# Optimization experiments

Measured on AMD Instinct MI355X. Metric: run time of the kernel, lower is better.

The kernel has to match this reference:

```python
import jax, jax.numpy as jnp
import numpy as np

ALPHA = 1.702
LIMIT = 7.0
BLOCK = 32  # mxfp4 block size (values per scale)

# fp4 e2m1 lookup table, indexed by 4-bit code (sign in high bit)
FP4_LUT = jnp.array([0.0, 0.5, 1.0, 1.5, 2.0, 3.0, 4.0, 6.0,
                     -0.0, -0.5, -1.0, -1.5, -2.0, -3.0, -4.0, -6.0],
                    dtype=jnp.float32)


def dequant_mxfp4(blocks, scales):
    # blocks: [E, R, C//2] int byte values (two fp4 nibbles per byte, low nibble first)
    # scales: [E, R, C//32] e8m0 exponents; value = 2^(scale - 127)
    E, R, _ = blocks.shape
    nb = scales.shape[-1]
    lo = blocks & 0xF
    hi = (blocks >> 4) & 0xF
    vals = jnp.stack([FP4_LUT[lo], FP4_LUT[hi]], axis=-1)  # [E,R,C//2,2]
    vals = vals.reshape(E, R, nb, BLOCK)
    scale = jnp.exp2((scales - 127).astype(jnp.float32))   # [E,R,nb]
    return (vals * scale[..., None]).reshape(E, R, nb * BLOCK)  # [E,R,C]


def setup_inputs() -> dict:
    key = jax.random.key(0)
    ks = jax.random.split(key, 12)
    T, E, H, I = 1024, 8, 1024, 1024
    inp = {
        'hidden_states': jax.random.normal(ks[0], (T, H), dtype=jnp.float32),
        'router_logits': jax.random.normal(ks[1], (T, E), dtype=jnp.float32),
        'gate_proj_blocks': jax.random.randint(ks[2], (E, I, H // 2), 0, 256, dtype=jnp.int32),
        'gate_proj_scales': jax.random.randint(ks[3], (E, I, H // BLOCK), 121, 130, dtype=jnp.int32),
        'gate_proj_bias': jax.random.normal(ks[4], (E, I), dtype=jnp.float32) * 0.02,
        'up_proj_blocks': jax.random.randint(ks[5], (E, I, H // 2), 0, 256, dtype=jnp.int32),
        'up_proj_scales': jax.random.randint(ks[6], (E, I, H // BLOCK), 121, 130, dtype=jnp.int32),
        'up_proj_bias': jax.random.normal(ks[7], (E, I), dtype=jnp.float32) * 0.02,
        'down_proj_blocks': jax.random.randint(ks[8], (E, H, I // 2), 0, 256, dtype=jnp.int32),
        'down_proj_scales': jax.random.randint(ks[9], (E, H, I // BLOCK), 121, 130, dtype=jnp.int32),
        'down_proj_bias': jax.random.normal(ks[10], (E, H), dtype=jnp.float32) * 0.02,
        'k': 2,
    }
    return inp


def reference(hidden_states, router_logits, gate_proj_blocks, gate_proj_scales,
              gate_proj_bias, up_proj_blocks, up_proj_scales, up_proj_bias,
              down_proj_blocks, down_proj_scales, down_proj_bias, k):
    T, H = hidden_states.shape
    E = router_logits.shape[-1]
    # --- top-k routing: softmax over the selected logits, scattered to [T,E] ---
    top_vals, top_idx = jax.lax.top_k(router_logits, k)        # [T,k]
    top_w = jax.nn.softmax(top_vals, axis=-1)                   # [T,k]
    route = jnp.zeros((T, E), dtype=hidden_states.dtype)
    route = route.at[jnp.arange(T)[:, None], top_idx].add(top_w)  # [T,E]
    # --- dequantize mxfp4 expert weights ---
    gate_w = dequant_mxfp4(gate_proj_blocks, gate_proj_scales)  # [E,I,H]
    up_w = dequant_mxfp4(up_proj_blocks, up_proj_scales)        # [E,I,H]
    down_w = dequant_mxfp4(down_proj_blocks, down_proj_scales)  # [E,H,I]
    # --- GLU expert FFN (GPT-OSS variant) ---
    gate = jnp.einsum('th,eih->tei', hidden_states, gate_w) + gate_proj_bias[None]
    up = jnp.einsum('th,eih->tei', hidden_states, up_w) + up_proj_bias[None]
    gate = jnp.minimum(gate, LIMIT)
    up = jnp.clip(up, -LIMIT, LIMIT)
    glu = gate * jax.nn.sigmoid(gate * ALPHA)
    act = (up + 1.0) * glu                                       # [T,E,I]
    # fold routing weight in before the down projection, then sum over experts
    act = act * route[:, :, None]
    out = jnp.einsum('tei,ehi->th', act, down_w) + route @ down_proj_bias  # [T,H]
    return out
```

## Files before the change

### kernel.cpp

```cpp
#include <hip/hip_runtime.h>
#include <cstdint>
#include <cstddef>

typedef __bf16 bf16x8 __attribute__((ext_vector_type(8)));
typedef __bf16 bf16x2 __attribute__((ext_vector_type(2)));
typedef float f32x4 __attribute__((ext_vector_type(4)));
typedef unsigned short u16x2 __attribute__((ext_vector_type(2)));

constexpr int HH = 1024;
constexpr int II = 1024;
constexpr int KMAX = 2;
constexpr int EMAX = 8;
constexpr int GU_TILES = 40;
constexpr int DN_TILES = 40;
constexpr float FALPHA = 1.702f;
constexpr float FLIMIT = 7.0f;

#if __has_builtin(__builtin_amdgcn_cvt_scalef32_pk_bf16_fp4)
#define USE_CVT 1
#else
#define USE_CVT 0
#endif

#define SCHED0() __builtin_amdgcn_sched_barrier(0)

__device__ __forceinline__ unsigned pk_add16(unsigned a, unsigned b) {
  u16x2 x, y;
  __builtin_memcpy(&x, &a, 4); __builtin_memcpy(&y, &b, 4);
  u16x2 r = x + y;
  unsigned o; __builtin_memcpy(&o, &r, 4); return o;
}
__device__ __forceinline__ int4 decode_chunk(int4 raw, unsigned addk) {
  unsigned p = (unsigned)raw.x | ((unsigned)raw.y << 8) |
               ((unsigned)raw.z << 16) | ((unsigned)raw.w << 24);
  unsigned q = p >> 4;
  unsigned me = p & 0x07070707u, mo = q & 0x07070707u;
  unsigned se = p & 0x08080808u, so = q & 0x08080808u;
  unsigned hiE = __builtin_amdgcn_perm(0x40404040u, 0x3F3F3F14u, me) | (se << 4);
  unsigned hiO = __builtin_amdgcn_perm(0x40404040u, 0x3F3F3F14u, mo) | (so << 4);
  unsigned loE = __builtin_amdgcn_perm(0xC0804000u, 0xC0800000u, me);
  unsigned loO = __builtin_amdgcn_perm(0xC0804000u, 0xC0800000u, mo);
  int4 out;
  out.x = (int)pk_add16(__builtin_amdgcn_perm(hiE, loE, 0x05010400u), addk);
  out.y = (int)pk_add16(__builtin_amdgcn_perm(hiE, loE, 0x07030602u), addk);
  out.z = (int)pk_add16(__builtin_amdgcn_perm(hiO, loO, 0x05010400u), addk);
  out.w = (int)pk_add16(__builtin_amdgcn_perm(hiO, loO, 0x07030602u), addk);
  return out;
}
__device__ __forceinline__ unsigned make_addk(int s) {
  int k = s - 127;
  unsigned t = ((unsigned)(k << 7)) & 0xFFFFu;
  return t | (t << 16);
}

__device__ __forceinline__ bf16x8 decode_frag(int4 raw, int s) {
#if USE_CVT
  unsigned t0 = __builtin_amdgcn_perm((unsigned)raw.y, (unsigned)raw.x, 0x00000400u);
  unsigned t1 = __builtin_amdgcn_perm((unsigned)raw.w, (unsigned)raw.z, 0x00000400u);
  unsigned p  = __builtin_amdgcn_perm(t1, t0, 0x05040100u);
  float scf = __uint_as_float((unsigned)s << 23);
  bf16x2 a = __builtin_amdgcn_cvt_scalef32_pk_bf16_fp4(p, scf, 0);
  bf16x2 b = __builtin_amdgcn_cvt_scalef32_pk_bf16_fp4(p, scf, 1);
  bf16x2 c = __builtin_amdgcn_cvt_scalef32_pk_bf16_fp4(p, scf, 2);
  bf16x2 d = __builtin_amdgcn_cvt_scalef32_pk_bf16_fp4(p, scf, 3);
  bf16x8 r;
  r[0]=a[0]; r[1]=a[1]; r[2]=b[0]; r[3]=b[1]; r[4]=c[0]; r[5]=c[1]; r[6]=d[0]; r[7]=d[1];
  return r;
#else
  int4 d4 = decode_chunk(raw, make_addk(s));
  bf16x8 r; __builtin_memcpy(&r, &d4, 16);
  return r;
#endif
}

__device__ __forceinline__ void gll16(const void* g, void* l) {
  __builtin_amdgcn_global_load_lds(
      (const __attribute__((address_space(1))) void*)g,
      (__attribute__((address_space(3))) void*)l, 16, 0, 0);
}

__device__ __forceinline__ int xcd_swz(int wg, int nwg) {
  int q = nwg >> 3, r = nwg & 7;
  int xcd = wg & 7, pos = wg >> 3;
  return (xcd < r ? xcd * (q + 1) : r * (q + 1) + (xcd - r) * q) + pos;
}

__global__ __launch_bounds__(1024) void prep_kernel(
    const float* __restrict__ logits, const int* __restrict__ dk, int T, int E,
    float* __restrict__ route, float* __restrict__ tw,
    int* __restrict__ lists, int* __restrict__ counts,
    int* __restrict__ tabGU, int* __restrict__ tabDN) {
  __shared__ unsigned char s_ti[1024];
  __shared__ int s_cnt[EMAX];
  int t = threadIdx.x;
  int kk = *dk; if (kk > KMAX) kk = KMAX; if (kk < 1) kk = 1;
  int EE = E > EMAX ? EMAX : E;
  if (t < T) {
    float v[EMAX]; bool used[EMAX];
    for (int e = 0; e < EE; ++e) { v[e] = logits[t * E + e]; used[e] = false; route[t * E + e] = 0.f; }
    float tv[KMAX]; int ti[KMAX];
    for (int j = 0; j < kk; ++j) {
      float best = -3.4e38f; int bi = 0;
      for (int e = 0; e < EE; ++e) if (!used[e] && v[e] > best) { best = v[e]; bi = e; }
      used[bi] = true; tv[j] = best; ti[j] = bi;
    }
    float mx = tv[0], ssum = 0.f, wj[KMAX];
    for (int j = 0; j < kk; ++j) { wj[j] = __expf(tv[j] - mx); ssum += wj[j]; }
    for (int j = 0; j < kk; ++j) {
      float wv = wj[j] / ssum;
      route[t * E + ti[j]] = wv;
      tw[t * kk + j] = wv;
    }
    s_ti[t] = (unsigned char)(ti[0] | ((kk > 1 ? ti[1] : 0xF) << 4));
  } else if (t < 1024) {
    s_ti[t] = 0xFF;
  }
  __syncthreads();
  int w = t >> 6, lane = t & 63;
  if (w < EE) {
    int e = w, cnt = 0;
    for (int base = 0; base < T; base += 64) {
      int tt = base + lane;
      int j = -1;
      if (tt < T) {
        int packed = s_ti[tt];
        if ((packed & 0xF) == e) j = 0;
        else if ((packed >> 4) == e) j = 1;
      }
      unsigned long long m = __ballot(j >= 0);
      if (j >= 0) {
        int pre = __popcll(m & ((1ull << lane) - 1ull));
        lists[e * T + cnt + pre] = (tt << 3) | j;
      }
      cnt += __popcll(m);
    }
    if (lane == 0) { counts[e] = cnt; s_cnt[e] = cnt; }
  }
  __syncthreads();
  if (t == 0) {
    int g = 0, d = 0;
    for (int e = 0; e < EE; ++e) {
      int c = s_cnt[e];
      for (int m = 0; m * 64 < c && g < GU_TILES; ++m) tabGU[g++] = (e << 16) | m;
      for (int m = 0; m * 64 < c && d < DN_TILES; ++m) tabDN[d++] = (e << 16) | m;
    }
    for (; g < GU_TILES; ++g) tabGU[g] = -1;
    for (; d < DN_TILES; ++d) tabDN[d] = -1;
  }
}

__global__ void convert_hs(const float* __restrict__ hs, __bf16* __restrict__ hsb, int n8) {
  int g = blockIdx.x * 256 + threadIdx.x;
  if (g >= n8) return;
  const float4* p = (const float4*)hs + (size_t)g * 2;
  float4 a = p[0], b = p[1];
  bf16x8 r;
#if USE_CVT
  r[0] = (__bf16)a.x; r[1] = (__bf16)a.y; r[2] = (__bf16)a.z; r[3] = (__bf16)a.w;
  r[4] = (__bf16)b.x; r[5] = (__bf16)b.y; r[6] = (__bf16)b.z; r[7] = (__bf16)b.w;
#else
  r[0] = (__bf16)a.x; r[1] = (__bf16)a.z; r[2] = (__bf16)b.x; r[3] = (__bf16)b.z;
  r[4] = (__bf16)a.y; r[5] = (__bf16)a.w; r[6] = (__bf16)b.y; r[7] = (__bf16)b.w;
#endif
  *(bf16x8*)(hsb + (size_t)g * 8) = r;
}

__global__ __launch_bounds__(128, 4) void gemm_gate_up(
    const __bf16* __restrict__ hsb,
    const int* __restrict__ gblk, const int* __restrict__ gscl, const float* __restrict__ gbias,
    const int* __restrict__ ublk, const int* __restrict__ uscl, const float* __restrict__ ubias,
    const int* __restrict__ lists, const int* __restrict__ counts,
    const float* __restrict__ tw, const int* __restrict__ dk,
    const int* __restrict__ tab,
    __bf16* __restrict__ act, int T)
{
  int lin = xcd_swz(blockIdx.x, GU_TILES * (II / 16));
  int ntile = lin / GU_TILES, xt = lin % GU_TILES;
  int te = tab[xt];
  if (te < 0) return;
  int e = te >> 16, mtile = te & 0xFFFF;
  int cnt = counts[e];
  int n_valid = cnt - mtile * 64;
  if (n_valid <= 0) return;
  if (n_valid > 64) n_valid = 64;
  int kk = *dk; if (kk > KMAX) kk = KMAX; if (kk < 1) kk = 1;
  int ibase = ntile * 16;

  __shared__ int s_tok[64];
  __shared__ __attribute__((aligned(16))) char Abuf[2][8192];
  __shared__ __attribute__((aligned(16))) char Braw[2][4096];
  __shared__ __attribute__((aligned(8))) unsigned short sS[32][36];

  int tid = threadIdx.x;
  if (tid < 64) {
    int idx = mtile * 64 + tid;
    s_tok[tid] = lists[e * T + (idx < cnt ? idx : mtile * 64)];
  }
  __syncthreads();

  int lane = tid & 63, w = tid >> 6;
  int r15 = lane & 15, kg = lane >> 4;
  int cA = (lane & 7) ^ ((lane >> 3) & 7);

  unsigned aOff[4];
  #pragma unroll
  for (int q = 0; q < 4; ++q) {
    int row = w * 32 + q * 8 + (lane >> 3);
    int tok = s_tok[row] >> 3;
    aOff[q] = (unsigned)tok * (HH * 2) + (unsigned)cA * 16;
  }
  const char* bSrc[2];
  #pragma unroll
  for (int q = 0; q < 2; ++q) {
    int row = w * 16 + q * 8 + (lane >> 3);
    int mat = (row >> 4) & 1;
    int i = ibase + (row & 15);
    const int* base = mat ? ublk : gblk;
    bSrc[q] = (const char*)(base + ((size_t)e * II + i) * (HH / 2)) + cA * 16;
  }

  #pragma unroll
  for (int q = 0; q < 4; ++q)
    gll16((const char*)hsb + aOff[q], Abuf[0] + (w * 32 + q * 8) * 128);
  #pragma unroll
  for (int q = 0; q < 2; ++q)
    gll16(bSrc[q], Braw[0] + (w * 16 + q * 8) * 128);
  #pragma unroll
  for (int q = 0; q < 4; ++q)
    gll16((const char*)hsb + aOff[q] + 128, Abuf[1] + (w * 32 + q * 8) * 128);
  #pragma unroll
  for (int q = 0; q < 2; ++q)
    gll16(bSrc[q] + 128, Braw[1] + (w * 16 + q * 8) * 128);

  for (int idx = tid; idx < 256; idx += 128) {
    int row = idx >> 3, c4 = idx & 7;
    int mat = (row >> 4) & 1;
    int i = ibase + (row & 15);
    const int* sbase = mat ? uscl : gscl;
    int4 v = *((const int4*)(sbase + ((size_t)e * II + i) * 32) + c4);
    unsigned short* dst = &sS[row][c4 * 4];
    dst[0] = (unsigned short)v.x; dst[1] = (unsigned short)v.y;
    dst[2] = (unsigned short)v.z; dst[3] = (unsigned short)v.w;
  }
  __syncthreads();

  f32x4 acc[2][2];
  #pragma unroll
  for (int a = 0; a < 2; ++a) { acc[a][0] = (f32x4)0.f; acc[a][1] = (f32x4)0.f; }

  constexpr int NK = HH / 64;
  #pragma unroll 1
  for (int t = 0; t < NK; ++t) {
    if (t > 0) {
      if (t < NK - 1) { asm volatile("s_waitcnt vmcnt(6)" ::: "memory"); }
      else            { asm volatile("s_waitcnt vmcnt(0)" ::: "memory"); }
      SCHED0();
      __builtin_amdgcn_s_barrier();
      SCHED0();
    }
    const char* Ac = Abuf[t & 1];
    const char* Bc = Braw[t & 1];
    unsigned sv[2];
    sv[0] = *(const unsigned*)((const char*)sS + (r15) * 72 + t * 4);
    sv[1] = *(const unsigned*)((const char*)sS + (16 + r15) * 72 + t * 4);
    #pragma unroll
    for (int kq = 0; kq < 2; ++kq) {
      int kc = kq * 4 + kg;
      bf16x8 bfr[2];
      #pragma unroll
      for (int fn = 0; fn < 2; ++fn) {
        int n = fn * 16 + r15;
        int4 raw = *(const int4*)(Bc + n * 128 + ((kc ^ (n & 7)) << 4));
        int s = kq ? (int)(sv[fn] >> 16) : (int)(sv[fn] & 0xFFFF);
        bfr[fn] = decode_frag(raw, s);
      }
      #pragma unroll
      for (int fm = 0; fm < 2; ++fm) {
        int m = w * 32 + fm * 16 + r15;
        bf16x8 af = *(const bf16x8*)(Ac + m * 128 + ((kc ^ (m & 7)) << 4));
        acc[fm][0] = __builtin_amdgcn_mfma_f32_16x16x32_bf16(af, bfr[0], acc[fm][0], 0, 0, 0);
        acc[fm][1] = __builtin_amdgcn_mfma_f32_16x16x32_bf16(af, bfr[1], acc[fm][1], 0, 0, 0);
      }
    }
    if (t + 2 < NK) {
      asm volatile("s_waitcnt lgkmcnt(0)" ::: "memory");
      SCHED0();
      __builtin_amdgcn_s_barrier();
      SCHED0();
      char* An = Abuf[t & 1];
      char* Bn = Braw[t & 1];
      #pragma unroll
      for (int q = 0; q < 4; ++q)
        gll16((const char*)hsb + aOff[q] + (t + 2) * 128, An + (w * 32 + q * 8) * 128);
      #pragma unroll
      for (int q = 0; q < 2; ++q)
        gll16(bSrc[q] + (t + 2) * 128, Bn + (w * 16 + q * 8) * 128);
    }
  }

  {
    int i_log = ibase + r15;
    float gb = gbias[e * II + i_log], ub = ubias[e * II + i_log];
#if USE_CVT
    int i_st = i_log;
#else
    int i_st = (i_log & ~7) | ((i_log & 1) << 2) | ((i_log & 7) >> 1);
#endif
    #pragma unroll
    for (int fm = 0; fm < 2; ++fm) {
      #pragma unroll
      for (int rg = 0; rg < 4; ++rg) {
        int mloc = w * 32 + fm * 16 + kg * 4 + rg;
        if (mloc < n_valid) {
          int entry = s_tok[mloc];
          int t2 = entry >> 3, j = entry & 7;
          float wv = tw[t2 * kk + j];
          float g = fminf(acc[fm][0][rg] + gb, FLIMIT);
          float u = fminf(fmaxf(acc[fm][1][rg] + ub, -FLIMIT), FLIMIT);
          float glu = g / (1.f + __expf(-FALPHA * g));
          act[((size_t)t2 * kk + j) * II + i_st] = (__bf16)((u + 1.f) * glu * wv);
        }
      }
    }
  }
}

__global__ __launch_bounds__(128, 4) void gemm_down(
    const __bf16* __restrict__ act,
    const int* __restrict__ dblk, const int* __restrict__ dscl,
    const int* __restrict__ lists, const int* __restrict__ counts,
    const int* __restrict__ dk, const int* __restrict__ tab,
    __bf16* __restrict__ partial, int T)
{
  int lin = xcd_swz(blockIdx.x, DN_TILES * (HH / 32));
  int ntile = lin / DN_TILES, xt = lin % DN_TILES;
  int te = tab[xt];
  if (te < 0) return;
  int e = te >> 16, mtile = te & 0xFFFF;
  int cnt = counts[e];
  int n_valid = cnt - mtile * 64;
  if (n_valid <= 0) return;
  if (n_valid > 64) n_valid = 64;
  int kk = *dk; if (kk > KMAX) kk = KMAX; if (kk < 1) kk = 1;
  int hbase = ntile * 32;

  __shared__ int s_tok[64];
  __shared__ __attribute__((aligned(16))) char Abuf[2][8192];
  __shared__ __attribute__((aligned(16))) char Braw[2][4096];
  __shared__ __attribute__((aligned(8))) unsigned short sS[32][36];

  int tid = threadIdx.x;
  if (tid < 64) {
    int idx = mtile * 64 + tid;
    s_tok[tid] = lists[e * T + (idx < cnt ? idx : mtile * 64)];
  }
  __syncthreads();

  int lane = tid & 63, w = tid >> 6;
  int r15 = lane & 15, kg = lane >> 4;
  int cA = (lane & 7) ^ ((lane >> 3) & 7);

  unsigned aOff[4];
  #pragma unroll
  for (int q = 0; q < 4; ++q) {
    int row = w * 32 + q * 8 + (lane >> 3);
    int entry = s_tok[row];
    unsigned slot = (unsigned)(entry >> 3) * kk + (entry & 7);
    aOff[q] = slot * (II * 2) + (unsigned)cA * 16;
  }
  const char* bSrc[2];
  #pragma unroll
  for (int q = 0; q < 2; ++q) {
    int row = w * 16 + q * 8 + (lane >> 3);
    bSrc[q] = (const char*)(dblk + ((size_t)e * HH + hbase + row) * (II / 2)) + cA * 16;
  }

  #pragma unroll
  for (int q = 0; q < 4; ++q)
    gll16((const char*)act + aOff[q], Abuf[0] + (w * 32 + q * 8) * 128);
  #pragma unroll
  for (int q = 0; q < 2; ++q)
    gll16(bSrc[q], Braw[0] + (w * 16 + q * 8) * 128);
  #pragma unroll
  for (int q = 0; q < 4; ++q)
    gll16((const char*)act + aOff[q] + 128, Abuf[1] + (w * 32 + q * 8) * 128);
  #pragma unroll
  for (int q = 0; q < 2; ++q)
    gll16(bSrc[q] + 128, Braw[1] + (w * 16 + q * 8) * 128);

  for (int idx = tid; idx < 256; idx += 128) {
    int row = idx >> 3, c4 = idx & 7;
    int4 v = *((const int4*)(dscl + ((size_t)e * HH + hbase + row) * 32) + c4);
    unsigned short* dst = &sS[row][c4 * 4];
    dst[0] = (unsigned short)v.x; dst[1] = (unsigned short)v.y;
    dst[2] = (unsigned short)v.z; dst[3] = (unsigned short)v.w;
  }
  __syncthreads();

  f32x4 acc[2][2];
  #pragma unroll
  for (int a = 0; a < 2; ++a) { acc[a][0] = (f32x4)0.f; acc[a][1] = (f32x4)0.f; }

  constexpr int NK = II / 64;
  #pragma unroll 1
  for (int t = 0; t < NK; ++t) {
    if (t > 0) {
      if (t < NK - 1) { asm volatile("s_waitcnt vmcnt(6)" ::: "memory"); }
      else            { asm volatile("s_waitcnt vmcnt(0)" ::: "memory"); }
      SCHED0();
      __builtin_amdgcn_s_barrier();
      SCHED0();
    }
    const char* Ac = Abuf[t & 1];
    const char* Bc = Braw[t & 1];
    unsigned sv[2];
    sv[0] = *(const unsigned*)((const char*)sS + (r15) * 72 + t * 4);
    sv[1] = *(const unsigned*)((const char*)sS + (16 + r15) * 72 + t * 4);
    #pragma unroll
    for (int kq = 0; kq < 2; ++kq) {
      int kc = kq * 4 + kg;
      bf16x8 bfr[2];
      #pragma unroll
      for (int fn = 0; fn < 2; ++fn) {
        int n = fn * 16 + r15;
        int4 raw = *(const int4*)(Bc + n * 128 + ((kc ^ (n & 7)) << 4));
        int s = kq ? (int)(sv[fn] >> 16) : (int)(sv[fn] & 0xFFFF);
        bfr[fn] = decode_frag(raw, s);
      }
      #pragma unroll
      for (int fm = 0; fm < 2; ++fm) {
        int m = w * 32 + fm * 16 + r15;
        bf16x8 af = *(const bf16x8*)(Ac + m * 128 + ((kc ^ (m & 7)) << 4));
        acc[fm][0] = __builtin_amdgcn_mfma_f32_16x16x32_bf16(af, bfr[0], acc[fm][0], 0, 0, 0);
        acc[fm][1] = __builtin_amdgcn_mfma_f32_16x16x32_bf16(af, bfr[1], acc[fm][1], 0, 0, 0);
      }
    }
    if (t + 2 < NK) {
      asm volatile("s_waitcnt lgkmcnt(0)" ::: "memory");
      SCHED0();
      __builtin_amdgcn_s_barrier();
      SCHED0();
      char* An = Abuf[t & 1];
      char* Bn = Braw[t & 1];
      #pragma unroll
      for (int q = 0; q < 4; ++q)
        gll16((const char*)act + aOff[q] + (t + 2) * 128, An + (w * 32 + q * 8) * 128);
      #pragma unroll
      for (int q = 0; q < 2; ++q)
        gll16(bSrc[q] + (t + 2) * 128, Bn + (w * 16 + q * 8) * 128);
    }
  }

  #pragma unroll
  for (int fm = 0; fm < 2; ++fm) {
    #pragma unroll
    for (int rg = 0; rg < 4; ++rg) {
      int mloc = w * 32 + fm * 16 + kg * 4 + rg;
      if (mloc < n_valid) {
        int entry = s_tok[mloc];
        int t2 = entry >> 3, j = entry & 7;
        size_t slot = (size_t)t2 * kk + j;
        #pragma unroll
        for (int fn = 0; fn < 2; ++fn) {
          int h = hbase + fn * 16 + r15;
          partial[slot * HH + h] = (__bf16)acc[fm][fn][rg];
        }
      }
    }
  }
}

__global__ void combine_kernel(const __bf16* __restrict__ partial, const float* __restrict__ route,
                               const float* __restrict__ dbias, const int* __restrict__ dk,
                               float* __restrict__ out, int E) {
  int t = blockIdx.y;
  int h = blockIdx.x * 256 + threadIdx.x;
  int kk = *dk; if (kk > KMAX) kk = KMAX; if (kk < 1) kk = 1;
  float s = 0.f;
  for (int j = 0; j < kk; ++j) s += (float)partial[((size_t)t * kk + j) * HH + h];
  for (int e = 0; e < E; ++e) s += route[t * E + e] * dbias[(size_t)e * HH + h];
  out[(size_t)t * HH + h] = s;
}

extern "C" void kernel_launch(void* const* d_in, const int* in_sizes, int n_in,
                              void* d_out, int out_size, void* d_ws, size_t ws_size,
                              hipStream_t stream) {
  const float* hs    = (const float*)d_in[0];
  const float* rl    = (const float*)d_in[1];
  const int*   gblk  = (const int*)d_in[2];
  const int*   gscl  = (const int*)d_in[3];
  const float* gbias = (const float*)d_in[4];
  const int*   ublk  = (const int*)d_in[5];
  const int*   uscl  = (const int*)d_in[6];
  const float* ubias = (const float*)d_in[7];
  const int*   dblk  = (const int*)d_in[8];
  const int*   dscl  = (const int*)d_in[9];
  const float* dbias = (const float*)d_in[10];
  const int*   dk    = (const int*)d_in[11];

  long s0 = in_sizes[0], s1 = in_sizes[1], s2 = in_sizes[2], s4 = in_sizes[4];
  int H = (int)(2 * s2 / s4);
  int T = (int)(s0 / H);
  int E = (int)(s1 / T);

  char* w = (char*)d_ws;
  auto alloc = [&](size_t bytes) { char* p = w; w += (bytes + 255) & ~size_t(255); return p; };
  float*  route   = (float*)alloc(sizeof(float) * (size_t)T * E);
  float*  twp     = (float*)alloc(sizeof(float) * (size_t)T * KMAX);
  int*    counts  = (int*)  alloc(sizeof(int)   * (size_t)E);
  int*    lists   = (int*)  alloc(sizeof(int)   * (size_t)E * T);
  int*    tabGU   = (int*)  alloc(sizeof(int)   * GU_TILES);
  int*    tabDN   = (int*)  alloc(sizeof(int)   * DN_TILES);
  __bf16* hsb     = (__bf16*)alloc(sizeof(__bf16) * (size_t)T * HH);
  __bf16* act     = (__bf16*)alloc(sizeof(__bf16) * (size_t)T * KMAX * II);
  __bf16* partial = (__bf16*)alloc(sizeof(__bf16) * (size_t)T * KMAX * HH);

  prep_kernel<<<dim3(1), 1024, 0, stream>>>(rl, dk, T, E, route, twp, lists, counts, tabGU, tabDN);
  convert_hs<<<dim3((T * HH / 8 + 255) / 256), 256, 0, stream>>>(hs, hsb, T * HH / 8);
  gemm_gate_up<<<dim3(GU_TILES * (II / 16)), 128, 0, stream>>>(
      hsb, gblk, gscl, gbias, ublk, uscl, ubias, lists, counts, twp, dk, tabGU, act, T);
  gemm_down<<<dim3(DN_TILES * (HH / 32)), 128, 0, stream>>>(
      act, dblk, dscl, lists, counts, dk, tabDN, partial, T);
  combine_kernel<<<dim3(HH / 256, T), 256, 0, stream>>>(partial, route, dbias, dk, (float*)d_out, E);
}
```

Baseline: 97.24 us.

## Use 32x32 MFMA with 64x64 tiles and fuse prep with hs conversion

Both expert GEMMs move from 16x16x32 MFMA with 64x32 (gate/up 64x16 per matrix) tiles to 32x32x16 MFMA with 64x64 tiles. Each weight row is decoded once and reused across two token halves, and the number of workgroups is halved. The gate/up epilogue pairs gate and up values across lanes with a shuffle. The routing prep kernel and the hidden-state bf16 conversion are merged into one launch to drop a kernel boundary. The barrier and waitcnt placement in the pipelined loop is also restructured. The trade-off is fewer blocks (less parallelism, occupancy hint lowered to 2) and a larger LDS footprint.

```diff
diff --git a/kernel.cpp b/kernel.cpp
--- a/kernel.cpp
+++ b/kernel.cpp
@@ -4,7 +4,7 @@
 
 typedef __bf16 bf16x8 __attribute__((ext_vector_type(8)));
 typedef __bf16 bf16x2 __attribute__((ext_vector_type(2)));
-typedef float f32x4 __attribute__((ext_vector_type(4)));
+typedef float f32x16 __attribute__((ext_vector_type(16)));
 typedef unsigned short u16x2 __attribute__((ext_vector_type(2)));
 
 constexpr int HH = 1024;
@@ -85,11 +85,29 @@
   return (xcd < r ? xcd * (q + 1) : r * (q + 1) + (xcd - r) * q) + pos;
 }
 
-__global__ __launch_bounds__(1024) void prep_kernel(
+__global__ __launch_bounds__(1024) void prep_convert(
     const float* __restrict__ logits, const int* __restrict__ dk, int T, int E,
     float* __restrict__ route, float* __restrict__ tw,
     int* __restrict__ lists, int* __restrict__ counts,
-    int* __restrict__ tabGU, int* __restrict__ tabDN) {
+    int* __restrict__ tabGU, int* __restrict__ tabDN,
+    const float* __restrict__ hs, __bf16* __restrict__ hsb, int n8) {
+  if ((int)blockIdx.x < (int)gridDim.x - 1) {
+    int g = blockIdx.x * 1024 + threadIdx.x;
+    if (g < n8) {
+      const float4* p = (const float4*)hs + (size_t)g * 2;
+      float4 a = p[0], b = p[1];
+      bf16x8 r;
+#if USE_CVT
+      r[0] = (__bf16)a.x; r[1] = (__bf16)a.y; r[2] = (__bf16)a.z; r[3] = (__bf16)a.w;
+      r[4] = (__bf16)b.x; r[5] = (__bf16)b.y; r[6] = (__bf16)b.z; r[7] = (__bf16)b.w;
+#else
+      r[0] = (__bf16)a.x; r[1] = (__bf16)a.z; r[2] = (__bf16)b.x; r[3] = (__bf16)b.z;
+      r[4] = (__bf16)a.y; r[5] = (__bf16)a.w; r[6] = (__bf16)b.y; r[7] = (__bf16)b.w;
+#endif
+      *(bf16x8*)(hsb + (size_t)g * 8) = r;
+    }
+    return;
+  }
   __shared__ unsigned char s_ti[1024];
   __shared__ int s_cnt[EMAX];
   int t = threadIdx.x;
@@ -149,23 +167,7 @@
   }
 }
 
-__global__ void convert_hs(const float* __restrict__ hs, __bf16* __restrict__ hsb, int n8) {
-  int g = blockIdx.x * 256 + threadIdx.x;
-  if (g >= n8) return;
-  const float4* p = (const float4*)hs + (size_t)g * 2;
-  float4 a = p[0], b = p[1];
-  bf16x8 r;
-#if USE_CVT
-  r[0] = (__bf16)a.x; r[1] = (__bf16)a.y; r[2] = (__bf16)a.z; r[3] = (__bf16)a.w;
-  r[4] = (__bf16)b.x; r[5] = (__bf16)b.y; r[6] = (__bf16)b.z; r[7] = (__bf16)b.w;
-#else
-  r[0] = (__bf16)a.x; r[1] = (__bf16)a.z; r[2] = (__bf16)b.x; r[3] = (__bf16)b.z;
-  r[4] = (__bf16)a.y; r[5] = (__bf16)a.w; r[6] = (__bf16)b.y; r[7] = (__bf16)b.w;
-#endif
-  *(bf16x8*)(hsb + (size_t)g * 8) = r;
-}
-
-__global__ __launch_bounds__(128, 4) void gemm_gate_up(
+__global__ __launch_bounds__(128, 2) void gemm_gate_up(
     const __bf16* __restrict__ hsb,
     const int* __restrict__ gblk, const int* __restrict__ gscl, const float* __restrict__ gbias,
     const int* __restrict__ ublk, const int* __restrict__ uscl, const float* __restrict__ ubias,
@@ -174,7 +176,7 @@
     const int* __restrict__ tab,
     __bf16* __restrict__ act, int T)
 {
-  int lin = xcd_swz(blockIdx.x, GU_TILES * (II / 16));
+  int lin = xcd_swz(blockIdx.x, GU_TILES * (II / 32));
   int ntile = lin / GU_TILES, xt = lin % GU_TILES;
   int te = tab[xt];
   if (te < 0) return;
@@ -184,12 +186,12 @@
   if (n_valid <= 0) return;
   if (n_valid > 64) n_valid = 64;
   int kk = *dk; if (kk > KMAX) kk = KMAX; if (kk < 1) kk = 1;
-  int ibase = ntile * 16;
+  int ibase = ntile * 32;
 
   __shared__ int s_tok[64];
   __shared__ __attribute__((aligned(16))) char Abuf[2][8192];
-  __shared__ __attribute__((aligned(16))) char Braw[2][4096];
-  __shared__ __attribute__((aligned(8))) unsigned short sS[32][36];
+  __shared__ __attribute__((aligned(16))) char Bbuf[2][8192];
+  __shared__ __attribute__((aligned(8))) unsigned short sS[64][36];
 
   int tid = threadIdx.x;
   if (tid < 64) {
@@ -199,107 +201,107 @@
   __syncthreads();
 
   int lane = tid & 63, w = tid >> 6;
-  int r15 = lane & 15, kg = lane >> 4;
-  int cA = (lane & 7) ^ ((lane >> 3) & 7);
-
-  unsigned aOff[4];
-  #pragma unroll
-  for (int q = 0; q < 4; ++q) {
-    int row = w * 32 + q * 8 + (lane >> 3);
+  int l31 = lane & 31, kg2 = lane >> 5;
+  int sub = lane >> 3, cL = lane & 7;
+  int cA = cL ^ (sub & 7);
+
+  const char* aSrc[4];
+  #pragma unroll
+  for (int q = 0; q < 4; ++q) {
+    int row = w * 32 + q * 8 + sub;
     int tok = s_tok[row] >> 3;
-    aOff[q] = (unsigned)tok * (HH * 2) + (unsigned)cA * 16;
-  }
-  const char* bSrc[2];
-  #pragma unroll
-  for (int q = 0; q < 2; ++q) {
-    int row = w * 16 + q * 8 + (lane >> 3);
+    aSrc[q] = (const char*)hsb + (size_t)tok * (HH * 2) + (size_t)cA * 16;
+  }
+  const char* bSrc[4];
+  #pragma unroll
+  for (int q = 0; q < 4; ++q) {
+    int row = w * 32 + q * 8 + sub;
     int mat = (row >> 4) & 1;
-    int i = ibase + (row & 15);
+    int i = ibase + ((row >> 5) << 4) + (row & 15);
     const int* base = mat ? ublk : gblk;
-    bSrc[q] = (const char*)(base + ((size_t)e * II + i) * (HH / 2)) + cA * 16;
-  }
-
-  #pragma unroll
-  for (int q = 0; q < 4; ++q)
-    gll16((const char*)hsb + aOff[q], Abuf[0] + (w * 32 + q * 8) * 128);
-  #pragma unroll
-  for (int q = 0; q < 2; ++q)
-    gll16(bSrc[q], Braw[0] + (w * 16 + q * 8) * 128);
-  #pragma unroll
-  for (int q = 0; q < 4; ++q)
-    gll16((const char*)hsb + aOff[q] + 128, Abuf[1] + (w * 32 + q * 8) * 128);
-  #pragma unroll
-  for (int q = 0; q < 2; ++q)
-    gll16(bSrc[q] + 128, Braw[1] + (w * 16 + q * 8) * 128);
-
-  for (int idx = tid; idx < 256; idx += 128) {
+    bSrc[q] = (const char*)(base + ((size_t)e * II + i) * (HH / 2)) + (size_t)cA * 16;
+  }
+
+  int4 sv4[4];
+  #pragma unroll
+  for (int rep = 0; rep < 4; ++rep) {
+    int idx = tid + rep * 128;
     int row = idx >> 3, c4 = idx & 7;
     int mat = (row >> 4) & 1;
-    int i = ibase + (row & 15);
+    int i = ibase + ((row >> 5) << 4) + (row & 15);
     const int* sbase = mat ? uscl : gscl;
-    int4 v = *((const int4*)(sbase + ((size_t)e * II + i) * 32) + c4);
+    sv4[rep] = *((const int4*)(sbase + ((size_t)e * II + i) * 32) + c4);
+  }
+  asm volatile("s_waitcnt vmcnt(0)" ::: "memory");
+  SCHED0();
+  #pragma unroll
+  for (int rep = 0; rep < 4; ++rep) {
+    int idx = tid + rep * 128;
+    int row = idx >> 3, c4 = idx & 7;
     unsigned short* dst = &sS[row][c4 * 4];
-    dst[0] = (unsigned short)v.x; dst[1] = (unsigned short)v.y;
-    dst[2] = (unsigned short)v.z; dst[3] = (unsigned short)v.w;
-  }
-  __syncthreads();
-
-  f32x4 acc[2][2];
-  #pragma unroll
-  for (int a = 0; a < 2; ++a) { acc[a][0] = (f32x4)0.f; acc[a][1] = (f32x4)0.f; }
+    dst[0] = (unsigned short)sv4[rep].x; dst[1] = (unsigned short)sv4[rep].y;
+    dst[2] = (unsigned short)sv4[rep].z; dst[3] = (unsigned short)sv4[rep].w;
+  }
+  #pragma unroll
+  for (int q = 0; q < 4; ++q) {
+    gll16(aSrc[q], Abuf[0] + (w * 32 + q * 8) * 128);
+    gll16(bSrc[q], Bbuf[0] + (w * 32 + q * 8) * 128);
+  }
+  #pragma unroll
+  for (int q = 0; q < 4; ++q) {
+    gll16(aSrc[q] + 128, Abuf[1] + (w * 32 + q * 8) * 128);
+    gll16(bSrc[q] + 128, Bbuf[1] + (w * 32 + q * 8) * 128);
+  }
+  asm volatile("s_waitcnt vmcnt(8)" ::: "memory");
+  asm volatile("s_waitcnt lgkmcnt(0)" ::: "memory");
+  SCHED0();
+  __builtin_amdgcn_s_barrier();
+  SCHED0();
+
+  f32x16 acc0 = (f32x16)0.f, acc1 = (f32x16)0.f;
+  int brow = w * 32 + l31;
 
   constexpr int NK = HH / 64;
   #pragma unroll 1
   for (int t = 0; t < NK; ++t) {
-    if (t > 0) {
-      if (t < NK - 1) { asm volatile("s_waitcnt vmcnt(6)" ::: "memory"); }
-      else            { asm volatile("s_waitcnt vmcnt(0)" ::: "memory"); }
-      SCHED0();
-      __builtin_amdgcn_s_barrier();
-      SCHED0();
-    }
     const char* Ac = Abuf[t & 1];
-    const char* Bc = Braw[t & 1];
-    unsigned sv[2];
-    sv[0] = *(const unsigned*)((const char*)sS + (r15) * 72 + t * 4);
-    sv[1] = *(const unsigned*)((const char*)sS + (16 + r15) * 72 + t * 4);
+    const char* Bc = Bbuf[t & 1];
+    unsigned sv = *(const unsigned*)((const char*)sS + brow * 72 + t * 4);
     #pragma unroll
-    for (int kq = 0; kq < 2; ++kq) {
-      int kc = kq * 4 + kg;
-      bf16x8 bfr[2];
+    for (int s = 0; s < 4; ++s) {
+      int kc = kg2 + 2 * s;
+      int4 rawb = *(const int4*)(Bc + brow * 128 + ((kc ^ (brow & 7)) << 4));
+      bf16x8 bb = decode_frag(rawb, (s >> 1) ? (int)(sv >> 16) : (int)(sv & 0xFFFF));
+      bf16x8 a0 = *(const bf16x8*)(Ac + l31 * 128 + ((kc ^ (l31 & 7)) << 4));
+      int m1 = l31 + 32;
+      bf16x8 a1 = *(const bf16x8*)(Ac + m1 * 128 + ((kc ^ (m1 & 7)) << 4));
+      acc0 = __builtin_amdgcn_mfma_f32_32x32x16_bf16(a0, bb, acc0, 0, 0, 0);
+      acc1 = __builtin_amdgcn_mfma_f32_32x32x16_bf16(a1, bb, acc1, 0, 0, 0);
+    }
+    asm volatile("s_waitcnt lgkmcnt(0)" ::: "memory");
+    SCHED0();
+    __builtin_amdgcn_s_barrier();
+    SCHED0();
+    if (t + 2 < NK) {
+      char* An = Abuf[t & 1];
+      char* Bn = Bbuf[t & 1];
       #pragma unroll
-      for (int fn = 0; fn < 2; ++fn) {
-        int n = fn * 16 + r15;
-        int4 raw = *(const int4*)(Bc + n * 128 + ((kc ^ (n & 7)) << 4));
-        int s = kq ? (int)(sv[fn] >> 16) : (int)(sv[fn] & 0xFFFF);
-        bfr[fn] = decode_frag(raw, s);
-      }
-      #pragma unroll
-      for (int fm = 0; fm < 2; ++fm) {
-        int m = w * 32 + fm * 16 + r15;
-        bf16x8 af = *(const bf16x8*)(Ac + m * 128 + ((kc ^ (m & 7)) << 4));
-        acc[fm][0] = __builtin_amdgcn_mfma_f32_16x16x32_bf16(af, bfr[0], acc[fm][0], 0, 0, 0);
-        acc[fm][1] = __builtin_amdgcn_mfma_f32_16x16x32_bf16(af, bfr[1], acc[fm][1], 0, 0, 0);
-      }
-    }
-    if (t + 2 < NK) {
-      asm volatile("s_waitcnt lgkmcnt(0)" ::: "memory");
-      SCHED0();
-      __builtin_amdgcn_s_barrier();
-      SCHED0();
-      char* An = Abuf[t & 1];
-      char* Bn = Braw[t & 1];
-      #pragma unroll
-      for (int q = 0; q < 4; ++q)
-        gll16((const char*)hsb + aOff[q] + (t + 2) * 128, An + (w * 32 + q * 8) * 128);
-      #pragma unroll
-      for (int q = 0; q < 2; ++q)
-        gll16(bSrc[q] + (t + 2) * 128, Bn + (w * 16 + q * 8) * 128);
-    }
+      for (int q = 0; q < 4; ++q) {
+        gll16(aSrc[q] + (t + 2) * 128, An + (w * 32 + q * 8) * 128);
+        gll16(bSrc[q] + (t + 2) * 128, Bn + (w * 32 + q * 8) * 128);
+      }
+      asm volatile("s_waitcnt vmcnt(8)" ::: "memory");
+    } else {
+      asm volatile("s_waitcnt vmcnt(0)" ::: "memory");
+    }
+    SCHED0();
+    __builtin_amdgcn_s_barrier();
+    SCHED0();
   }
 
   {
-    int i_log = ibase + r15;
+    bool isGate = (l31 & 16) == 0;
+    int i_log = ibase + w * 16 + (l31 & 15);
     float gb = gbias[e * II + i_log], ub = ubias[e * II + i_log];
 #if USE_CVT
     int i_st = i_log;
@@ -307,32 +309,46 @@
     int i_st = (i_log & ~7) | ((i_log & 1) << 2) | ((i_log & 7) >> 1);
 #endif
     #pragma unroll
-    for (int fm = 0; fm < 2; ++fm) {
-      #pragma unroll
-      for (int rg = 0; rg < 4; ++rg) {
-        int mloc = w * 32 + fm * 16 + kg * 4 + rg;
-        if (mloc < n_valid) {
-          int entry = s_tok[mloc];
-          int t2 = entry >> 3, j = entry & 7;
-          float wv = tw[t2 * kk + j];
-          float g = fminf(acc[fm][0][rg] + gb, FLIMIT);
-          float u = fminf(fmaxf(acc[fm][1][rg] + ub, -FLIMIT), FLIMIT);
-          float glu = g / (1.f + __expf(-FALPHA * g));
-          act[((size_t)t2 * kk + j) * II + i_st] = (__bf16)((u + 1.f) * glu * wv);
-        }
-      }
-    }
-  }
-}
-
-__global__ __launch_bounds__(128, 4) void gemm_down(
+    for (int r = 0; r < 16; ++r) {
+      float gv = acc0[r];
+      float ov = __shfl_xor(gv, 16);
+      int row = (r & 3) + 8 * (r >> 2) + 4 * kg2;
+      if (isGate && row < n_valid) {
+        int entry = s_tok[row];
+        int t2 = entry >> 3, j = entry & 7;
+        float wv = tw[t2 * kk + j];
+        float g = fminf(gv + gb, FLIMIT);
+        float u = fminf(fmaxf(ov + ub, -FLIMIT), FLIMIT);
+        float glu = g / (1.f + __expf(-FALPHA * g));
+        act[((size_t)t2 * kk + j) * II + i_st] = (__bf16)((u + 1.f) * glu * wv);
+      }
+    }
+    #pragma unroll
+    for (int r = 0; r < 16; ++r) {
+      float gv = acc1[r];
+      float ov = __shfl_xor(gv, 16);
+      int row = (r & 3) + 8 * (r >> 2) + 4 * kg2 + 32;
+      if (isGate && row < n_valid) {
+        int entry = s_tok[row];
+        int t2 = entry >> 3, j = entry & 7;
+        float wv = tw[t2 * kk + j];
+        float g = fminf(gv + gb, FLIMIT);
+        float u = fminf(fmaxf(ov + ub, -FLIMIT), FLIMIT);
+        float glu = g / (1.f + __expf(-FALPHA * g));
+        act[((size_t)t2 * kk + j) * II + i_st] = (__bf16)((u + 1.f) * glu * wv);
+      }
+    }
+  }
+}
+
+__global__ __launch_bounds__(128, 2) void gemm_down(
     const __bf16* __restrict__ act,
     const int* __restrict__ dblk, const int* __restrict__ dscl,
     const int* __restrict__ lists, const int* __restrict__ counts,
     const int* __restrict__ dk, const int* __restrict__ tab,
     __bf16* __restrict__ partial, int T)
 {
-  int lin = xcd_swz(blockIdx.x, DN_TILES * (HH / 32));
+  int lin = xcd_swz(blockIdx.x, DN_TILES * (HH / 64));
   int ntile = lin / DN_TILES, xt = lin % DN_TILES;
   int te = tab[xt];
   if (te < 0) return;
@@ -342,12 +358,12 @@
   if (n_valid <= 0) return;
   if (n_valid > 64) n_valid = 64;
   int kk = *dk; if (kk > KMAX) kk = KMAX; if (kk < 1) kk = 1;
-  int hbase = ntile * 32;
+  int hbase = ntile * 64;
 
   __shared__ int s_tok[64];
   __shared__ __attribute__((aligned(16))) char Abuf[2][8192];
-  __shared__ __attribute__((aligned(16))) char Braw[2][4096];
-  __shared__ __attribute__((aligned(8))) unsigned short sS[32][36];
+  __shared__ __attribute__((aligned(16))) char Bbuf[2][8192];
+  __shared__ __attribute__((aligned(8))) unsigned short sS[64][36];
 
   int tid = threadIdx.x;
   if (tid < 64) {
@@ -357,114 +373,117 @@
   __syncthreads();
 
   int lane = tid & 63, w = tid >> 6;
-  int r15 = lane & 15, kg = lane >> 4;
-  int cA = (lane & 7) ^ ((lane >> 3) & 7);
-
-  unsigned aOff[4];
-  #pragma unroll
-  for (int q = 0; q < 4; ++q) {
-    int row = w * 32 + q * 8 + (lane >> 3);
+  int l31 = lane & 31, kg2 = lane >> 5;
+  int sub = lane >> 3, cL = lane & 7;
+  int cA = cL ^ (sub & 7);
+
+  const char* aSrc[4];
+  #pragma unroll
+  for (int q = 0; q < 4; ++q) {
+    int row = w * 32 + q * 8 + sub;
     int entry = s_tok[row];
-    unsigned slot = (unsigned)(entry >> 3) * kk + (entry & 7);
-    aOff[q] = slot * (II * 2) + (unsigned)cA * 16;
-  }
-  const char* bSrc[2];
-  #pragma unroll
-  for (int q = 0; q < 2; ++q) {
-    int row = w * 16 + q * 8 + (lane >> 3);
-    bSrc[q] = (const char*)(dblk + ((size_t)e * HH + hbase + row) * (II / 2)) + cA * 16;
-  }
-
-  #pragma unroll
-  for (int q = 0; q < 4; ++q)
-    gll16((const char*)act + aOff[q], Abuf[0] + (w * 32 + q * 8) * 128);
-  #pragma unroll
-  for (int q = 0; q < 2; ++q)
-    gll16(bSrc[q], Braw[0] + (w * 16 + q * 8) * 128);
-  #pragma unroll
-  for (int q = 0; q < 4; ++q)
-    gll16((const char*)act + aOff[q] + 128, Abuf[1] + (w * 32 + q * 8) * 128);
-  #pragma unroll
-  for (int q = 0; q < 2; ++q)
-    gll16(bSrc[q] + 128, Braw[1] + (w * 16 + q * 8) * 128);
-
-  for (int idx = tid; idx < 256; idx += 128) {
+    size_t slot = (size_t)(entry >> 3) * kk + (entry & 7);
+    aSrc[q] = (const char*)act + slot * (II * 2) + (size_t)cA * 16;
+  }
+  const char* bSrc[4];
+  #pragma unroll
+  for (int q = 0; q < 4; ++q) {
+    int row = w * 32 + q * 8 + sub;
+    bSrc[q] = (const char*)(dblk + ((size_t)e * HH + hbase + row) * (II / 2)) + (size_t)cA * 16;
+  }
+
+  int4 sv4[4];
+  #pragma unroll
+  for (int rep = 0; rep < 4; ++rep) {
+    int idx = tid + rep * 128;
     int row = idx >> 3, c4 = idx & 7;
-    int4 v = *((const int4*)(dscl + ((size_t)e * HH + hbase + row) * 32) + c4);
+    sv4[rep] = *((const int4*)(dscl + ((size_t)e * HH + hbase + row) * 32) + c4);
+  }
+  asm volatile("s_waitcnt vmcnt(0)" ::: "memory");
+  SCHED0();
+  #pragma unroll
+  for (int rep = 0; rep < 4; ++rep) {
+    int idx = tid + rep * 128;
+    int row = idx >> 3, c4 = idx & 7;
     unsigned short* dst = &sS[row][c4 * 4];
-    dst[0] = (unsigned short)v.x; dst[1] = (unsigned short)v.y;
-    dst[2] = (unsigned short)v.z; dst[3] = (unsigned short)v.w;
-  }
-  __syncthreads();
-
-  f32x4 acc[2][2];
-  #pragma unroll
-  for (int a = 0; a < 2; ++a) { acc[a][0] = (f32x4)0.f; acc[a][1] = (f32x4)0.f; }
+    dst[0] = (unsigned short)sv4[rep].x; dst[1] = (unsigned short)sv4[rep].y;
+    dst[2] = (unsigned short)sv4[rep].z; dst[3] = (unsigned short)sv4[rep].w;
+  }
+  #pragma unroll
+  for (int q = 0; q < 4; ++q) {
+    gll16(aSrc[q], Abuf[0] + (w * 32 + q * 8) * 128);
+    gll16(bSrc[q], Bbuf[0] + (w * 32 + q * 8) * 128);
+  }
+  #pragma unroll
+  for (int q = 0; q < 4; ++q) {
+    gll16(aSrc[q] + 128, Abuf[1] + (w * 32 + q * 8) * 128);
+    gll16(bSrc[q] + 128, Bbuf[1] + (w * 32 + q * 8) * 128);
+  }
+  asm volatile("s_waitcnt vmcnt(8)" ::: "memory");
+  asm volatile("s_waitcnt lgkmcnt(0)" ::: "memory");
+  SCHED0();
+  __builtin_amdgcn_s_barrier();
+  SCHED0();
+
+  f32x16 acc0 = (f32x16)0.f, acc1 = (f32x16)0.f;
+  int brow = w * 32 + l31;
 
   constexpr int NK = II / 64;
   #pragma unroll 1
   for (int t = 0; t < NK; ++t) {
-    if (t > 0) {
-      if (t < NK - 1) { asm volatile("s_waitcnt vmcnt(6)" ::: "memory"); }
-      else            { asm volatile("s_waitcnt vmcnt(0)" ::: "memory"); }
-      SCHED0();
-      __builtin_amdgcn_s_barrier();
-      SCHED0();
-    }
     const char* Ac = Abuf[t & 1];
-    const char* Bc = Braw[t & 1];
-    unsigned sv[2];
-    sv[0] = *(const unsigned*)((const char*)sS + (r15) * 72 + t * 4);
-    sv[1] = *(const unsigned*)((const char*)sS + (16 + r15) * 72 + t * 4);
+    const char* Bc = Bbuf[t & 1];
+    unsigned sv = *(const unsigned*)((const char*)sS + brow * 72 + t * 4);
     #pragma unroll
-    for (int kq = 0; kq < 2; ++kq) {
-      int kc = kq * 4 + kg;
-      bf16x8 bfr[2];
+    for (int s = 0; s < 4; ++s) {
+      int kc = kg2 + 2 * s;
+      int4 rawb = *(const int4*)(Bc + brow * 128 + ((kc ^ (brow & 7)) << 4));
+      bf16x8 bb = decode_frag(rawb, (s >> 1) ? (int)(sv >> 16) : (int)(sv & 0xFFFF));
+      bf16x8 a0 = *(const bf16x8*)(Ac + l31 * 128 + ((kc ^ (l31 & 7)) << 4));
+      int m1 = l31 + 32;
+      bf16x8 a1 = *(const bf16x8*)(Ac + m1 * 128 + ((kc ^ (m1 & 7)) << 4));
+      acc0 = __builtin_amdgcn_mfma_f32_32x32x16_bf16(a0, bb, acc0, 0, 0, 0);
+      acc1 = __builtin_amdgcn_mfma_f32_32x32x16_bf16(a1, bb, acc1, 0, 0, 0);
+    }
+    asm volatile("s_waitcnt lgkmcnt(0)" ::: "memory");
+    SCHED0();
+    __builtin_amdgcn_s_barrier();
+    SCHED0();
+    if (t + 2 < NK) {
+      char* An = Abuf[t & 1];
+      char* Bn = Bbuf[t & 1];
       #pragma unroll
-      for (int fn = 0; fn < 2; ++fn) {
-        int n = fn * 16 + r15;
-        int4 raw = *(const int4*)(Bc + n * 128 + ((kc ^ (n & 7)) << 4));
-        int s = kq ? (int)(sv[fn] >> 16) : (int)(sv[fn] & 0xFFFF);
-        bfr[fn] = decode_frag(raw, s);
-      }
-      #pragma unroll
-      for (int fm = 0; fm < 2; ++fm) {
-        int m = w * 32 + fm * 16 + r15;
-        bf16x8 af = *(const bf16x8*)(Ac + m * 128 + ((kc ^ (m & 7)) << 4));
-        acc[fm][0] = __builtin_amdgcn_mfma_f32_16x16x32_bf16(af, bfr[0], acc[fm][0], 0, 0, 0);
-        acc[fm][1] = __builtin_amdgcn_mfma_f32_16x16x32_bf16(af, bfr[1], acc[fm][1], 0, 0, 0);
-      }
-    }
-    if (t + 2 < NK) {
-      asm volatile("s_waitcnt lgkmcnt(0)" ::: "memory");
-      SCHED0();
-      __builtin_amdgcn_s_barrier();
-      SCHED0();
-      char* An = Abuf[t & 1];
-      char* Bn = Braw[t & 1];
-      #pragma unroll
-      for (int q = 0; q < 4; ++q)
-        gll16((const char*)act + aOff[q] + (t + 2) * 128, An + (w * 32 + q * 8) * 128);
-      #pragma unroll
-      for (int q = 0; q < 2; ++q)
-        gll16(bSrc[q] + (t + 2) * 128, Bn + (w * 16 + q * 8) * 128);
-    }
-  }
-
-  #pragma unroll
-  for (int fm = 0; fm < 2; ++fm) {
+      for (int q = 0; q < 4; ++q) {
+        gll16(aSrc[q] + (t + 2) * 128, An + (w * 32 + q * 8) * 128);
+        gll16(bSrc[q] + (t + 2) * 128, Bn + (w * 32 + q * 8) * 128);
+      }
+      asm volatile("s_waitcnt vmcnt(8)" ::: "memory");
+    } else {
+      asm volatile("s_waitcnt vmcnt(0)" ::: "memory");
+    }
+    SCHED0();
+    __builtin_amdgcn_s_barrier();
+    SCHED0();
+  }
+
+  {
+    int h = hbase + w * 32 + l31;
     #pragma unroll
-    for (int rg = 0; rg < 4; ++rg) {
-      int mloc = w * 32 + fm * 16 + kg * 4 + rg;
-      if (mloc < n_valid) {
-        int entry = s_tok[mloc];
+    for (int r = 0; r < 16; ++r) {
+      int row = (r & 3) + 8 * (r >> 2) + 4 * kg2;
+      if (row < n_valid) {
+        int entry = s_tok[row];
         int t2 = entry >> 3, j = entry & 7;
-        size_t slot = (size_t)t2 * kk + j;
-        #pragma unroll
-        for (int fn = 0; fn < 2; ++fn) {
-          int h = hbase + fn * 16 + r15;
-          partial[slot * HH + h] = (__bf16)acc[fm][fn][rg];
-        }
+        partial[((size_t)t2 * kk + j) * HH + h] = (__bf16)acc0[r];
+      }
+    }
+    #pragma unroll
+    for (int r = 0; r < 16; ++r) {
+      int row = (r & 3) + 8 * (r >> 2) + 4 * kg2 + 32;
+      if (row < n_valid) {
+        int entry = s_tok[row];
+        int t2 = entry >> 3, j = entry & 7;
+        partial[((size_t)t2 * kk + j) * HH + h] = (__bf16)acc1[r];
       }
     }
   }
@@ -515,11 +534,13 @@
   __bf16* act     = (__bf16*)alloc(sizeof(__bf16) * (size_t)T * KMAX * II);
   __bf16* partial = (__bf16*)alloc(sizeof(__bf16) * (size_t)T * KMAX * HH);
 
-  prep_kernel<<<dim3(1), 1024, 0, stream>>>(rl, dk, T, E, route, twp, lists, counts, tabGU, tabDN);
-  convert_hs<<<dim3((T * HH / 8 + 255) / 256), 256, 0, stream>>>(hs, hsb, T * HH / 8);
-  gemm_gate_up<<<dim3(GU_TILES * (II / 16)), 128, 0, stream>>>(
+  int n8 = T * HH / 8;
+  int nConv = (n8 + 1023) / 1024;
+  prep_convert<<<dim3(nConv + 1), 1024, 0, stream>>>(
+      rl, dk, T, E, route, twp, lists, counts, tabGU, tabDN, hs, hsb, n8);
+  gemm_gate_up<<<dim3(GU_TILES * (II / 32)), 128, 0, stream>>>(
       hsb, gblk, gscl, gbias, ublk, uscl, ubias, lists, counts, twp, dk, tabGU, act, T);
-  gemm_down<<<dim3(DN_TILES * (HH / 32)), 128, 0, stream>>>(
+  gemm_down<<<dim3(DN_TILES * (HH / 64)), 128, 0, stream>>>(
       act, dblk, dscl, lists, counts, dk, tabDN, partial, T);
   combine_kernel<<<dim3(HH / 256, T), 256, 0, stream>>>(partial, route, dbias, dk, (float*)d_out, E);
 }
```

After: 106.2 us. 1.09x slower.
